# Kernel tuning notes

Measured on AMD Instinct MI355X. Metric: run time of the kernel, lower is better.

Reference implementation:

```python
import jax, jax.numpy as jnp
import numpy as np

BIT = 8      # shared-exponent mantissa bits (bf_conf.*_bit)
GSZ = 36     # block size (bf_conf.*_sz)


def bfp_quantize(x, bit=BIT, sz=GSZ):
    """Block floating point: groups of `sz` consecutive elements share one
    exponent e = floor(log2(max|x|)); each element keeps `bit` mantissa bits."""
    shape = x.shape
    flat = x.reshape(-1)
    n = flat.shape[0]
    pad = (-n) % sz
    flat = jnp.pad(flat, (0, pad))
    g = flat.reshape(-1, sz)                                   # [G, sz]
    maxabs = jnp.max(jnp.abs(g), axis=1, keepdims=True)
    e = jnp.floor(jnp.log2(jnp.where(maxabs > 0, maxabs, 1.0)))
    scale = jnp.exp2(e - (bit - 1))                            # lsb of shared-exp format
    q = jnp.round(g / scale) * scale
    q = jnp.where(maxabs > 0, q, 0.0)
    return q.reshape(-1)[:n].reshape(shape)


def setup_inputs() -> dict:
    key = jax.random.key(0)
    k1, k2, k3 = jax.random.split(key, 3)
    B, Cin, Cout, H, W, K = 16, 32, 32, 224, 224, 3
    x = jax.random.normal(k1, (B, Cin, H, W), dtype=jnp.float32)
    fan_in = Cin * K * K
    bound = 1.0 / np.sqrt(fan_in)
    weight = jax.random.uniform(k2, (Cout, Cin, K, K), jnp.float32, -bound, bound)
    bias = jax.random.uniform(k3, (Cout,), jnp.float32, -bound, bound)
    return {"x": x, "weight": weight, "bias": bias}


def reference(x, weight, bias):
    xq = bfp_quantize(x)          # f_i
    wq = bfp_quantize(weight)     # f_w
    out = jax.lax.conv_general_dilated(
        xq, wq,
        window_strides=(1, 1),
        padding=((1, 1), (1, 1)),
        rhs_dilation=(1, 1),
        feature_group_count=1,
        dimension_numbers=("NCHW", "OIHW", "NCHW"),
    )
    out = out + bias[None, :, None, None]
    out = bfp_quantize(out)       # f_o
    return out
```

## Files before the change

### kernel.cpp

```cpp
#include <hip/hip_runtime.h>
#include <hip/hip_bf16.h>

#define GSZ 36
static const int NX  = 16 * 32 * 224 * 224;
static const int NX4 = NX / 4;
static const int NW  = 32 * 32 * 3 * 3;
static const int GXN = (NX + GSZ - 1) / GSZ;
static const int HWp = 224 * 224;

typedef short bf16x8 __attribute__((ext_vector_type(8)));
typedef float f32x4  __attribute__((ext_vector_type(4)));

__device__ __forceinline__ unsigned div36(unsigned n) {
    return (unsigned)(((unsigned long long)n * 954437177ull) >> 35);
}
__device__ __forceinline__ float scale_from_max(float m) {
    int e = (int)((__float_as_uint(m) >> 23) & 0xffu) - 127;
    return __uint_as_float((unsigned)(e + 120) << 23);
}
__device__ __forceinline__ float inv_from_scale(float s) {
    return __uint_as_float(0x7F000000u - __float_as_uint(s));
}
__device__ __forceinline__ unsigned short f2bf(float f) {
    return (unsigned short)(__float_as_uint(f) >> 16);
}

__global__ void k_quant_wt(const float* __restrict__ w, unsigned short* __restrict__ wt) {
    int g = threadIdx.x;
    int base = g * GSZ;
    float v[GSZ];
    const float4* p = reinterpret_cast<const float4*>(w + base);
    #pragma unroll
    for (int i = 0; i < 9; ++i) {
        float4 t = p[i];
        v[4*i+0] = t.x; v[4*i+1] = t.y; v[4*i+2] = t.z; v[4*i+3] = t.w;
    }
    float m = 0.0f;
    #pragma unroll
    for (int i = 0; i < GSZ; ++i) m = fmaxf(m, fabsf(v[i]));
    if (m > 0.0f) {
        float s = scale_from_max(m), inv = inv_from_scale(s);
        #pragma unroll
        for (int i = 0; i < GSZ; ++i) v[i] = rintf(v[i] * inv) * s;
    }
    #pragma unroll
    for (int i = 0; i < GSZ; ++i) {
        int f = base + i;
        int co = f / 288, rem = f - co * 288;
        int ci = rem / 9, s = rem - ci * 9;
        wt[s * 1024 + co * 32 + ci] = f2bf(v[i]);
    }
}

#define TSTR 452
__global__ __launch_bounds__(256, 4) void k_quant_x_fused(const float* __restrict__ x,
                                                          unsigned short* __restrict__ xt) {
    __shared__ __align__(16) unsigned short tile[32 * TSTR];
    __shared__ float pmax[16 * 128];
    __shared__ float scl[32 * 14];

    int t = threadIdx.x;
    int b = blockIdx.y, hp = blockIdx.x;
    int F0 = (b * 32) * HWp + hp * 448;

    int c4  = t & 127;
    int ciB = t >> 7;
    int gi4 = (c4 * 57) >> 9;

    #pragma unroll
    for (int h = 0; h < 2; ++h) {
        f32x4 v[8];
        #pragma unroll
        for (int j = 0; j < 8; ++j) {
            int cl = ciB + 2 * j;
            int ci = h * 16 + cl;
            int F = F0 + ci * HWp;
            int r = F - 36 * (int)div36((unsigned)F);
            int f4 = (int)(((unsigned)(F - r)) >> 2) + c4;
            f32x4 tv = {0.f, 0.f, 0.f, 0.f};
            if ((unsigned)f4 < (unsigned)NX4)
                tv = reinterpret_cast<const f32x4*>(x)[f4];
            v[j] = tv;
            pmax[cl * 128 + c4] = fmaxf(fmaxf(fabsf(tv[0]), fabsf(tv[1])),
                                        fmaxf(fabsf(tv[2]), fabsf(tv[3])));
        }
        __syncthreads();

        if (t < 224) {
            int cl = (t * 2341) >> 15;
            int gi = t - cl * 14;
            const float* pp = &pmax[cl * 128 + 9 * gi];
            float m = pp[0];
            #pragma unroll
            for (int i = 1; i < 9; ++i) m = fmaxf(m, pp[i]);
            scl[(h * 16 + cl) * 14 + gi] = (m > 0.f) ? scale_from_max(m) : 0.f;
        }
        __syncthreads();

        #pragma unroll
        for (int j = 0; j < 8; ++j) {
            int ci = h * 16 + ciB + 2 * j;
            int F = F0 + ci * HWp;
            int r = F - 36 * (int)div36((unsigned)F);
            int rel = 4 * c4 - r;
            if ((unsigned)rel < 448u) {
                float s = scl[ci * 14 + gi4];
                f32x4 q = v[j];
                if (s > 0.f) {
                    float inv = inv_from_scale(s);
                    #pragma unroll
                    for (int k = 0; k < 4; ++k) q[k] = rintf(q[k] * inv) * s;
                } else {
                    q = f32x4{0.f, 0.f, 0.f, 0.f};
                }
                uint2 o;
                o.x = (unsigned)f2bf(q[0]) | ((unsigned)f2bf(q[1]) << 16);
                o.y = (unsigned)f2bf(q[2]) | ((unsigned)f2bf(q[3]) << 16);
                *reinterpret_cast<uint2*>(&tile[ci * TSTR + rel]) = o;
            }
        }
        __syncthreads();
    }

    unsigned short* ob = xt + ((size_t)b * HWp + hp * 448) * 32;
    for (int j = 0; j < 7; ++j) {
        int qd = t + 256 * j;
        int px = qd >> 2;
        int c0 = (qd & 3) * 8;
        unsigned uu[4];
        #pragma unroll
        for (int p = 0; p < 4; ++p) {
            unsigned short lo = tile[(c0 + 2 * p) * TSTR + px];
            unsigned short hi = tile[(c0 + 2 * p + 1) * TSTR + px];
            uu[p] = (unsigned)lo | ((unsigned)hi << 16);
        }
        *reinterpret_cast<uint4*>(ob + (size_t)px * 32 + c0) =
            make_uint4(uu[0], uu[1], uu[2], uu[3]);
    }
}

#define PXS 40
#define COS 452
__global__ __launch_bounds__(256, 2) void k_conv_q(const unsigned short* __restrict__ xt,
                                                   const unsigned short* __restrict__ wt,
                                                   const float* __restrict__ bias,
                                                   float* __restrict__ out) {
    __shared__ __align__(16) unsigned char lraw[4 * 226 * PXS * 2];
    unsigned short* xs = reinterpret_cast<unsigned short*>(lraw);
    float* ot = reinterpret_cast<float*>(lraw);
    __shared__ float scl[32 * 12];
    __shared__ int rel0s[32], bnds[32];

    int tid  = threadIdx.x;
    int lane = tid & 63;
    int wid  = tid >> 6;
    int hpair = blockIdx.x;
    int b     = blockIdx.y;
    int h0 = hpair * 2;

    if (tid < 32) {
        int T = (b * 32 + tid) * HWp + hpair * 448;
        int r36 = T - 36 * (int)div36((unsigned)T);
        int rel0 = r36 ? 36 - r36 : 0;
        rel0s[tid] = rel0;
        bnds[tid] = rel0 + 36 * (int)div36((unsigned)(448 - rel0));
    }

    const unsigned short* xb = xt + (size_t)b * HWp * 32;
    for (int k = 0; k < 15; ++k) {
        int q = tid + k * 256;
        if (q < 3616) {
            int r = ((q >> 3) * 145) >> 14;
            int rem = q - r * 904;
            int p = rem >> 2, ch = rem & 3;
            int gh = h0 - 1 + r, gw = p - 1;
            uint4 val = make_uint4(0u, 0u, 0u, 0u);
            if ((unsigned)gh < 224u && (unsigned)gw < 224u)
                val = *reinterpret_cast<const uint4*>(xb + ((size_t)(gh * 224 + gw)) * 32 + ch * 8);
            *reinterpret_cast<uint4*>(&xs[(r * 226 + p) * PXS + ch * 8]) = val;
        }
    }

    bf16x8 Wf[9][2];
    #pragma unroll
    for (int s = 0; s < 9; ++s)
        #pragma unroll
        for (int hf = 0; hf < 2; ++hf)
            Wf[s][hf] = *reinterpret_cast<const bf16x8*>(
                wt + s * 1024 + (hf * 16 + (lane & 15)) * 32 + (lane >> 4) * 8);

    int m4 = (lane >> 4) << 2;
    f32x4 acc[7][2];
    {
        f32x4 b0, b1;
        #pragma unroll
        for (int r = 0; r < 4; ++r) {
            b0[r] = bias[m4 + r];
            b1[r] = bias[16 + m4 + r];
        }
        #pragma unroll
        for (int i = 0; i < 7; ++i) { acc[i][0] = b0; acc[i][1] = b1; }
    }

    __syncthreads();

    int l15 = lane & 15;
    int kchunk = (lane >> 4) << 3;
    #pragma unroll
    for (int s = 0; s < 9; ++s) {
        int kh = s / 3, kw = s - kh * 3;
        #pragma unroll
        for (int i = 0; i < 7; ++i) {
            int f = wid * 7 + i;
            int row = (f >= 14) ? 1 : 0;
            int colf = (f - 14 * row) << 4;
            bf16x8 X = *reinterpret_cast<const bf16x8*>(
                &xs[((row + kh) * 226 + colf + l15 + kw) * PXS + kchunk]);
            acc[i][0] = __builtin_amdgcn_mfma_f32_16x16x32_bf16(Wf[s][0], X, acc[i][0], 0, 0, 0);
            acc[i][1] = __builtin_amdgcn_mfma_f32_16x16x32_bf16(Wf[s][1], X, acc[i][1], 0, 0, 0);
        }
    }
    __syncthreads();

    #pragma unroll
    for (int i = 0; i < 7; ++i) {
        int f = wid * 7 + i;
        int row = (f >= 14) ? 1 : 0;
        int px = row * 224 + ((f - 14 * row) << 4) + l15;
        #pragma unroll
        for (int hf = 0; hf < 2; ++hf)
            #pragma unroll
            for (int r = 0; r < 4; ++r)
                ot[(hf * 16 + m4 + r) * COS + px] = acc[i][hf][r];
    }
    __syncthreads();

    #pragma unroll
    for (int it = 0; it < 2; ++it) {
        int task = tid + it * 256;
        if (task < 384) {
            int co = ((task >> 2) * 683) >> 11;
            int k = task - co * 12;
            int base = rel0s[co] + 36 * k;
            if (base < bnds[co]) {
                const float* pp = &ot[co * COS + base];
                float m = 0.f;
                #pragma unroll
                for (int i = 0; i < 9; ++i) {
                    f32x4 vv = *reinterpret_cast<const f32x4*>(pp + 4 * i);
                    m = fmaxf(m, fmaxf(fmaxf(fabsf(vv[0]), fabsf(vv[1])),
                                       fmaxf(fabsf(vv[2]), fabsf(vv[3]))));
                }
                scl[co * 12 + k] = (m > 0.f) ? scale_from_max(m) : 0.f;
            }
        }
    }
    __syncthreads();

    float* ob = out + (size_t)(b * 32) * HWp + h0 * 224;
    #pragma unroll
    for (int j = 0; j < 14; ++j) {
        int idx = tid + j * 256;
        int co = ((idx >> 4) * 2341) >> 14;
        int c4 = idx - co * 112;
        int px0 = c4 * 4;
        f32x4 v = *reinterpret_cast<const f32x4*>(&ot[co * COS + px0]);
        int rz = px0 - rel0s[co];
        if ((unsigned)rz < (unsigned)(bnds[co] - rel0s[co])) {
            int k = (int)div36((unsigned)rz);
            float s = scl[co * 12 + k];
            if (s > 0.f) {
                float inv = inv_from_scale(s);
                #pragma unroll
                for (int e = 0; e < 4; ++e) v[e] = rintf(v[e] * inv) * s;
            } else {
                v = f32x4{0.f, 0.f, 0.f, 0.f};
            }
        }
        *reinterpret_cast<f32x4*>(ob + (size_t)co * HWp + px0) = v;
    }
}

__global__ __launch_bounds__(256) void k_fixup(float* __restrict__ buf) {
    int i = blockIdx.x * 256 + threadIdx.x;
    if (i >= 50976) return;
    const unsigned long long SP =
        12ull | (24ull << 7) | (37ull << 14) | (49ull << 21) |
        (62ull << 28) | (74ull << 35) | (87ull << 42) | (99ull << 49);
    int g = (i >> 3) * 112 + (int)((SP >> (7 * (i & 7))) & 127ull);
    if (g >= GXN) return;
    int f4 = 9 * g;
    f32x4 v[9];
    float m = 0.f;
    #pragma unroll
    for (int k = 0; k < 9; ++k) {
        f32x4 tv = {0.f, 0.f, 0.f, 0.f};
        if ((unsigned)(f4 + k) < (unsigned)NX4)
            tv = reinterpret_cast<const f32x4*>(buf)[f4 + k];
        v[k] = tv;
        m = fmaxf(m, fmaxf(fmaxf(fabsf(tv[0]), fabsf(tv[1])),
                           fmaxf(fabsf(tv[2]), fabsf(tv[3]))));
    }
    if (m > 0.f) {
        float s = scale_from_max(m), inv = inv_from_scale(s);
        #pragma unroll
        for (int k = 0; k < 9; ++k) {
            #pragma unroll
            for (int e = 0; e < 4; ++e) v[k][e] = rintf(v[k][e] * inv) * s;
            if ((unsigned)(f4 + k) < (unsigned)NX4)
                reinterpret_cast<f32x4*>(buf)[f4 + k] = v[k];
        }
    }
}

extern "C" void kernel_launch(void* const* d_in, const int* in_sizes, int n_in,
                              void* d_out, int out_size, void* d_ws, size_t ws_size,
                              hipStream_t stream) {
    (void)in_sizes; (void)n_in; (void)out_size; (void)ws_size;
    const float* x    = (const float*)d_in[0];
    const float* w    = (const float*)d_in[1];
    const float* bias = (const float*)d_in[2];
    float* out        = (float*)d_out;

    unsigned short* xt = (unsigned short*)d_ws;
    unsigned short* wt = xt + NX;

    k_quant_wt<<<1, 256, 0, stream>>>(w, wt);
    k_quant_x_fused<<<dim3(112, 16), 256, 0, stream>>>(x, xt);
    k_conv_q<<<dim3(112, 16), 256, 0, stream>>>(xt, wt, bias, out);
    k_fixup<<<200, 256, 0, stream>>>(out);
}
```

Measured before the change: 247.7 us.

## Fuse weight quantization into x-quant kernel, widen LDS transpose reads, remap conv blocks

Weight quantization moves into block (0,0) of the activation quantization kernel, which removes one kernel launch. The transpose write-out now reads 32-bit pairs from LDS and emits two pixels per task, so it issues fewer LDS reads. The conv kernel gets a remapped block order that spreads consecutive blocks across XCDs for L2 locality. Block (0,0) now does extra serial work, which could lengthen the tail of that kernel.

```diff
diff --git a/kernel.cpp b/kernel.cpp
--- a/kernel.cpp
+++ b/kernel.cpp
@@ -25,36 +25,11 @@
     return (unsigned short)(__float_as_uint(f) >> 16);
 }
 
-__global__ void k_quant_wt(const float* __restrict__ w, unsigned short* __restrict__ wt) {
-    int g = threadIdx.x;
-    int base = g * GSZ;
-    float v[GSZ];
-    const float4* p = reinterpret_cast<const float4*>(w + base);
-    #pragma unroll
-    for (int i = 0; i < 9; ++i) {
-        float4 t = p[i];
-        v[4*i+0] = t.x; v[4*i+1] = t.y; v[4*i+2] = t.z; v[4*i+3] = t.w;
-    }
-    float m = 0.0f;
-    #pragma unroll
-    for (int i = 0; i < GSZ; ++i) m = fmaxf(m, fabsf(v[i]));
-    if (m > 0.0f) {
-        float s = scale_from_max(m), inv = inv_from_scale(s);
-        #pragma unroll
-        for (int i = 0; i < GSZ; ++i) v[i] = rintf(v[i] * inv) * s;
-    }
-    #pragma unroll
-    for (int i = 0; i < GSZ; ++i) {
-        int f = base + i;
-        int co = f / 288, rem = f - co * 288;
-        int ci = rem / 9, s = rem - ci * 9;
-        wt[s * 1024 + co * 32 + ci] = f2bf(v[i]);
-    }
-}
-
 #define TSTR 452
 __global__ __launch_bounds__(256, 4) void k_quant_x_fused(const float* __restrict__ x,
-                                                          unsigned short* __restrict__ xt) {
+                                                          unsigned short* __restrict__ xt,
+                                                          const float* __restrict__ w,
+                                                          unsigned short* __restrict__ wt) {
     __shared__ __align__(16) unsigned short tile[32 * TSTR];
     __shared__ float pmax[16 * 128];
     __shared__ float scl[32 * 14];
@@ -123,19 +98,52 @@
     }
 
     unsigned short* ob = xt + ((size_t)b * HWp + hp * 448) * 32;
-    for (int j = 0; j < 7; ++j) {
-        int qd = t + 256 * j;
-        int px = qd >> 2;
-        int c0 = (qd & 3) * 8;
-        unsigned uu[4];
-        #pragma unroll
-        for (int p = 0; p < 4; ++p) {
-            unsigned short lo = tile[(c0 + 2 * p) * TSTR + px];
-            unsigned short hi = tile[(c0 + 2 * p + 1) * TSTR + px];
-            uu[p] = (unsigned)lo | ((unsigned)hi << 16);
-        }
-        *reinterpret_cast<uint4*>(ob + (size_t)px * 32 + c0) =
-            make_uint4(uu[0], uu[1], uu[2], uu[3]);
+    for (int j = 0; j < 4; ++j) {
+        int task = t + 256 * j;
+        if (task < 896) {
+            int px0 = (task >> 2) << 1;
+            int c0 = (task & 3) * 8;
+            unsigned r[8];
+            #pragma unroll
+            for (int p = 0; p < 8; ++p)
+                r[p] = *reinterpret_cast<const unsigned*>(&tile[(c0 + p) * TSTR + px0]);
+            unsigned ua[4], ub[4];
+            #pragma unroll
+            for (int p = 0; p < 4; ++p) {
+                ua[p] = (r[2*p] & 0xffffu) | (r[2*p+1] << 16);
+                ub[p] = (r[2*p] >> 16)     | (r[2*p+1] & 0xffff0000u);
+            }
+            *reinterpret_cast<uint4*>(ob + (size_t)px0 * 32 + c0) =
+                make_uint4(ua[0], ua[1], ua[2], ua[3]);
+            *reinterpret_cast<uint4*>(ob + (size_t)(px0 + 1) * 32 + c0) =
+                make_uint4(ub[0], ub[1], ub[2], ub[3]);
+        }
+    }
+
+    if (b == 0 && hp == 0) {
+        int base = t * GSZ;
+        float vw[GSZ];
+        const float4* p = reinterpret_cast<const float4*>(w + base);
+        #pragma unroll
+        for (int i = 0; i < 9; ++i) {
+            float4 tv = p[i];
+            vw[4*i+0] = tv.x; vw[4*i+1] = tv.y; vw[4*i+2] = tv.z; vw[4*i+3] = tv.w;
+        }
+        float m = 0.0f;
+        #pragma unroll
+        for (int i = 0; i < GSZ; ++i) m = fmaxf(m, fabsf(vw[i]));
+        if (m > 0.0f) {
+            float s = scale_from_max(m), inv = inv_from_scale(s);
+            #pragma unroll
+            for (int i = 0; i < GSZ; ++i) vw[i] = rintf(vw[i] * inv) * s;
+        }
+        #pragma unroll
+        for (int i = 0; i < GSZ; ++i) {
+            int f = base + i;
+            int co = f / 288, rem = f - co * 288;
+            int ci = rem / 9, s = rem - ci * 9;
+            wt[s * 1024 + co * 32 + ci] = f2bf(vw[i]);
+        }
     }
 }
 
@@ -154,8 +162,10 @@
     int tid  = threadIdx.x;
     int lane = tid & 63;
     int wid  = tid >> 6;
-    int hpair = blockIdx.x;
-    int b     = blockIdx.y;
+    int flat = blockIdx.y * 112 + blockIdx.x;
+    int nf = (flat & 7) * 224 + (flat >> 3);
+    int b     = nf / 112;
+    int hpair = nf - b * 112;
     int h0 = hpair * 2;
 
     if (tid < 32) {
@@ -325,8 +335,7 @@
     unsigned short* xt = (unsigned short*)d_ws;
     unsigned short* wt = xt + NX;
 
-    k_quant_wt<<<1, 256, 0, stream>>>(w, wt);
-    k_quant_x_fused<<<dim3(112, 16), 256, 0, stream>>>(x, xt);
+    k_quant_x_fused<<<dim3(112, 16), 256, 0, stream>>>(x, xt, w, wt);
     k_conv_q<<<dim3(112, 16), 256, 0, stream>>>(xt, wt, bias, out);
     k_fixup<<<200, 256, 0, stream>>>(out);
 }
```

New measurement: 241.8 us. 2.4% less time.
